# Kernel optimization log

Hardware: AMD Instinct MI355X
Metric: run time of the kernel (lower is better)

The kernel has to match this reference:

```python
import jax, jax.numpy as jnp
import numpy as np

DIM = 128
B, NQ, NK = 4, 4096, 4096
SCALE = DIM ** -0.5


def setup_inputs() -> dict:
    key = jax.random.key(0)
    ks = jax.random.split(key, 13)
    def lin(k, shape, scale=0.02):
        return jax.random.normal(k, shape, dtype=jnp.float32) * scale
    return {
        "query": jax.random.normal(ks[0], (B, NQ, DIM), dtype=jnp.float32),
        "key": jax.random.normal(ks[1], (B, NK, DIM), dtype=jnp.float32),
        "value": jax.random.normal(ks[2], (B, NK, DIM), dtype=jnp.float32),
        "att_bias": jax.random.normal(ks[3], (B, NK), dtype=jnp.float32),
        # params, [in, out] layout (torch Linear is x @ W.T + b)
        "q_w": lin(ks[4], (DIM, DIM)), "q_b": jnp.zeros((DIM,), jnp.float32),
        "k_w": lin(ks[5], (DIM, DIM)),
        "v_w": lin(ks[6], (DIM, DIM)), "v_b": jnp.zeros((DIM,), jnp.float32),
        "vs_w": lin(ks[7], (DIM, 1)), "vs_b": jnp.zeros((1,), jnp.float32),
        "p_w": lin(ks[8], (DIM, DIM)), "p_b": jnp.zeros((DIM,), jnp.float32),
    }


def reference(query, key, value, att_bias, q_w, q_b, k_w, v_w, v_b, vs_w, vs_b, p_w, p_b):
    # projections
    q = query @ q_w + q_b                      # [B, NQ, D]
    k = key @ k_w                              # [B, NK, D] (no bias)
    v = value @ v_w + v_b                      # [B, NK, D]
    # per-key semantic scalar, broadcast over queries: [B, 1, NK]
    semantic = (value @ vs_w + vs_b).reshape(value.shape[0], 1, value.shape[1])
    # scores + biases
    attn = jnp.einsum('bqd,bkd->bqk', q, k) * SCALE + semantic
    attn = attn + att_bias[:, None, :]
    attn = jax.nn.softmax(attn, axis=-1)
    out = jnp.einsum('bqk,bkd->bqd', attn, v)  # [B, NQ, D]
    out = out @ p_w + p_b
    return out
```

## Files before the change

### kernel.cpp

```cpp
#include <hip/hip_runtime.h>

typedef __bf16 bf16x8 __attribute__((ext_vector_type(8)));
typedef float f32x4 __attribute__((ext_vector_type(4)));
typedef float f32x16 __attribute__((ext_vector_type(16)));

#define MFMA16(a,b,c) __builtin_amdgcn_mfma_f32_16x16x32_bf16(a,b,c,0,0,0)
#define MFMA32(a,b,c) __builtin_amdgcn_mfma_f32_32x32x16_bf16(a,b,c,0,0,0)

static __device__ __forceinline__ unsigned short f2bf(float f){
  union{float f;unsigned u;}v; v.f=f;
  unsigned u=v.u;
  u += 0x7fffu + ((u>>16)&1u);
  return (unsigned short)(u>>16);
}
static __device__ __forceinline__ float bf2f(unsigned short h){
  union{unsigned u;float f;}v; v.u=((unsigned)h)<<16; return v.f;
}
static __device__ __forceinline__ unsigned cvtpk(float lo, float hi){
  unsigned r;
  asm("v_cvt_pk_bf16_f32 %0, %1, %2" : "=v"(r) : "v"(lo), "v"(hi));
  return r;
}
static __device__ __forceinline__ void gload16(const void* g, void* l){
  __builtin_amdgcn_global_load_lds(
    (const __attribute__((address_space(1))) unsigned int*)(uintptr_t)g,
    (__attribute__((address_space(3))) unsigned int*)(uintptr_t)l,
    16, 0, 0);
}

#define SCALE_QK 0.08838834764831845f
#define LOG2E    1.44269504088896340f
#define THR_L2   11.541560327111708f

#define SWZ128(r,c) (((r)<<7) + ((c) ^ (((r)&7)<<3)))


__global__ __launch_bounds__(256) void k_proj(
    const float* __restrict__ query, const float* __restrict__ key,
    const float* __restrict__ value, const float* __restrict__ att_bias,
    const float* __restrict__ q_w, const float* __restrict__ q_b,
    const float* __restrict__ k_w, const float* __restrict__ v_w,
    const float* __restrict__ v_b, const float* __restrict__ vs_w,
    const float* __restrict__ vs_b,
    unsigned short* __restrict__ qp, unsigned short* __restrict__ kp,
    unsigned short* __restrict__ vpt, float* __restrict__ biasc)
{
  const int t = blockIdx.y;
  const float* X = (t==0) ? query : ((t==1) ? key : value);
  const float* W = (t==0) ? q_w  : ((t==1) ? k_w : v_w);
  const int tid = threadIdx.x;
  const int row0 = blockIdx.x * 64;

  __shared__ __align__(16) unsigned short Wt[128][136];
  __shared__ __align__(16) unsigned short Xs[64][136];
  __shared__ float vsw_s[128];

  #pragma unroll 4
  for (int i=0;i<16;i++){
    int idx = tid*64 + i*4;
    float4 v4 = *(const float4*)(W + idx);
    Wt[(idx+0)&127][(idx+0)>>7] = f2bf(v4.x);
    Wt[(idx+1)&127][(idx+1)>>7] = f2bf(v4.y);
    Wt[(idx+2)&127][(idx+2)>>7] = f2bf(v4.z);
    Wt[(idx+3)&127][(idx+3)>>7] = f2bf(v4.w);
  }
  {
    const float* Xb = X + (size_t)row0*128;
    #pragma unroll
    for (int i=0;i<8;i++){
      int f4 = i*256 + tid;
      int row = f4>>5, c4 = f4&31;
      float4 v = *(const float4*)(Xb + row*128 + c4*4);
      ushort4 h;
      h.x = f2bf(v.x); h.y = f2bf(v.y); h.z = f2bf(v.z); h.w = f2bf(v.w);
      *(ushort4*)&Xs[row][c4*4] = h;
    }
  }
  if (t==2 && tid<128) vsw_s[tid] = vs_w[tid];
  __syncthreads();

  const int w = tid>>6, lane = tid&63, lr = lane&15, lg = lane>>4;
  f32x4 acc[8];
  #pragma unroll
  for (int nt=0;nt<8;nt++) acc[nt] = (f32x4){0.f,0.f,0.f,0.f};
  #pragma unroll
  for (int kk=0;kk<4;kk++){
    bf16x8 a = *(const bf16x8*)&Xs[w*16+lr][kk*32+lg*8];
    #pragma unroll
    for (int nt=0;nt<8;nt++){
      bf16x8 bb = *(const bf16x8*)&Wt[nt*16+lr][kk*32+lg*8];
      acc[nt] = MFMA16(a,bb,acc[nt]);
    }
  }

  if (t < 2){
    const float* bias = (t==0) ? q_b : (const float*)nullptr;
    const float sc = (t==0) ? (SCALE_QK*LOG2E) : 1.f;
    unsigned short* dstm = (t==0) ? qp : kp;
    #pragma unroll
    for (int nt=0;nt<8;nt++){
      int col = nt*16+lr;
      float bv = bias ? bias[col] : 0.f;
      #pragma unroll
      for (int r=0;r<4;r++){
        int row = row0 + w*16 + lg*4 + r;
        dstm[(size_t)row*128+col] = f2bf((acc[nt][r] + bv) * sc);
      }
    }
  } else {
    {
      int rl = tid>>2, part = tid&3;
      float s = 0.f;
      #pragma unroll
      for (int j=0;j<32;j++){
        int d = part*32+j;
        s += bf2f(Xs[rl][d]) * vsw_s[d];
      }
      s += __shfl_xor(s,1);
      s += __shfl_xor(s,2);
      if ((tid&3)==0){
        int rg = row0 + rl;
        biasc[rg] = (s + vs_b[0] + att_bias[rg]) * LOG2E;
      }
    }
    __syncthreads();
    unsigned short* Vls = (unsigned short*)Wt;
    #pragma unroll
    for (int nt=0;nt<8;nt++){
      int col = nt*16+lr;
      float bv = v_b[col];
      #pragma unroll
      for (int r=0;r<4;r++){
        int rl_ = w*16 + lg*4 + r;
        int k5 = rl_ & 31;
        int pos = 16*(k5>>4) + (k5&3) + 4*((k5>>3)&1) + 8*((k5>>2)&1);
        int np = (rl_ & 32) | pos;
        Vls[col*72 + np] = f2bf(acc[nt][r] + bv);
      }
    }
    __syncthreads();
    int d = tid>>1, half = tid&1;
    int bi = row0>>12, n0 = row0&4095;
    unsigned short* dst = vpt + ((size_t)(bi*128+d))*4096 + n0 + half*32;
    const unsigned short* src = Vls + d*72 + half*32;
    #pragma unroll
    for (int i=0;i<4;i++)
      *(uint4*)(dst + i*8) = *(const uint4*)(src + i*8);
  }
}

__global__ __launch_bounds__(256,3) void k_flash(
    const unsigned short* __restrict__ qp, const unsigned short* __restrict__ kp,
    const unsigned short* __restrict__ vpt, const float* __restrict__ biasc,
    unsigned short* __restrict__ opart, float* __restrict__ ml)
{
  const int f = blockIdx.x;
  const int xcd = f & 7, slot = f >> 3;
  const int group = xcd*4 + (slot>>5);
  const int b = group>>3, split = group&7;
  const int q0 = (slot & 31) * 128;

  const int tid = threadIdx.x;
  const int w = tid>>6, lane = tid&63;
  const int l31 = lane&31, hi = lane>>5;

  __shared__ __align__(16) unsigned short Ks[2][32*128];
  __shared__ __align__(16) char Vp[2][8192];
  __shared__ __align__(16) float Bs[512];

  const unsigned short* kbase = kp  + (size_t)(b*4096 + split*512)*128;
  const char* vbase = (const char*)(vpt + (size_t)b*128*4096 + split*512);
  const float* bbase = biasc + b*4096 + split*512;

  if (w < 2) gload16(bbase + w*256 + lane*4, (char*)Bs + w*1024);

  bf16x8 qf[8];
  {
    const unsigned short* qrow = qp + ((size_t)(b*4096 + q0 + w*32 + l31))*128;
    #pragma unroll
    for (int kk=0;kk<8;kk++) qf[kk] = *(const bf16x8*)(qrow + kk*16 + hi*8);
  }

  #define STAGE(bf_, k0_) do{                                                 \
    const char* kb_ = (const char*)kbase + (size_t)(k0_)*256;                 \
    const char* vb_ = vbase + (size_t)(k0_)*2;                                \
    _Pragma("unroll")                                                         \
    for (int i=0;i<2;i++){                                                    \
      int s_ = w*2+i;                                                         \
      int kr = s_*4 + (lane>>4);                                              \
      gload16(kb_ + kr*256 + (((lane&15)*16) ^ ((kr&7)*16)),                  \
              (char*)Ks[bf_] + s_*1024);                                      \
      int u_ = (lane&7) ^ ((lane>>3)&7);                                      \
      int vd = s_*16 + ((lane>>3)<<1) + (u_>>2);                              \
      gload16(vb_ + (size_t)vd*8192 + ((u_&3)<<4),                            \
              (char*)Vp[bf_] + s_*1024);                                      \
    }                                                                         \
  }while(0)

  float m_run = -INFINITY, l_run = 0.f;
  f32x16 acc[4];
  #pragma unroll
  for (int dt=0;dt<4;dt++) acc[dt] = (f32x16){};

  STAGE(0, 0);
  __syncthreads();

  const int vA = (l31>>1)*128;
  const int vX = ((l31>>1)&7)<<4;
  const int vH = (l31&1)*64 + hi*16;

  for (int t=0;t<16;t++){
    const int cur = t & 1;
    if (t<15) STAGE(cur^1, (t+1)*32);

    const unsigned short* Kc = Ks[cur];
    const char* Vc = Vp[cur];

    f32x16 sc = {};
    __builtin_amdgcn_s_setprio(1);
    #pragma unroll
    for (int kk=0;kk<8;kk++){
      bf16x8 a = *(const bf16x8*)&Kc[SWZ128(l31, kk*16 + hi*8)];
      sc = MFMA32(a, qf[kk], sc);
    }
    __builtin_amdgcn_s_setprio(0);

    const float* Bt = &Bs[t*32];
    float4 b0 = *(const float4*)&Bt[hi*4];
    float4 b1 = *(const float4*)&Bt[8 + hi*4];
    float4 b2 = *(const float4*)&Bt[16 + hi*4];
    float4 b3 = *(const float4*)&Bt[24 + hi*4];
    float tmax = -1e30f;
    #pragma unroll
    for (int c=0;c<4;c++){
      sc[c]    += ((const float*)&b0)[c];
      sc[4+c]  += ((const float*)&b1)[c];
      sc[8+c]  += ((const float*)&b2)[c];
      sc[12+c] += ((const float*)&b3)[c];
    }
    #pragma unroll
    for (int i=0;i<16;i++) tmax = fmaxf(tmax, sc[i]);
    tmax = fmaxf(tmax, __shfl_xor(tmax, 32));

    if (!__all(tmax <= m_run + THR_L2)){
      float mn = fmaxf(m_run, tmax);
      float corr = __builtin_exp2f(m_run - mn);
      m_run = mn;
      l_run *= corr;
      #pragma unroll
      for (int r=0;r<16;r++){
        int qn = (r&3) + 8*(r>>2) + 4*hi;
        float ca = __shfl(corr, qn);
        acc[0][r]*=ca; acc[1][r]*=ca; acc[2][r]*=ca; acc[3][r]*=ca;
      }
    }

    float rs = 0.f;
    #pragma unroll
    for (int i=0;i<16;i++){
      sc[i] = __builtin_exp2f(sc[i]-m_run); rs += sc[i];
    }
    rs += __shfl_xor(rs, 32);
    l_run += rs;

    {
      union { unsigned u[4]; bf16x8 v; } pu0;
      pu0.u[0] = cvtpk(sc[0], sc[1]);
      pu0.u[1] = cvtpk(sc[2], sc[3]);
      pu0.u[2] = cvtpk(sc[4], sc[5]);
      pu0.u[3] = cvtpk(sc[6], sc[7]);
      __builtin_amdgcn_s_setprio(1);
      #pragma unroll
      for (int dt=0;dt<4;dt++){
        bf16x8 v0 = *(const bf16x8*)(Vc + dt*2048 + vA + ((vH +  0) ^ vX));
        acc[dt] = MFMA32(pu0.v, v0, acc[dt]);
      }
      __builtin_amdgcn_s_setprio(0);
    }
    {
      union { unsigned u[4]; bf16x8 v; } pu1;
      pu1.u[0] = cvtpk(sc[8],  sc[9]);
      pu1.u[1] = cvtpk(sc[10], sc[11]);
      pu1.u[2] = cvtpk(sc[12], sc[13]);
      pu1.u[3] = cvtpk(sc[14], sc[15]);
      __builtin_amdgcn_s_setprio(1);
      #pragma unroll
      for (int dt=0;dt<4;dt++){
        bf16x8 v1 = *(const bf16x8*)(Vc + dt*2048 + vA + ((vH + 32) ^ vX));
        acc[dt] = MFMA32(pu1.v, v1, acc[dt]);
      }
      __builtin_amdgcn_s_setprio(0);
    }

    __syncthreads();
  }
  #undef STAGE

  const size_t rowbase = (size_t)split*16384 + (size_t)b*4096 + q0;
  #pragma unroll
  for (int r=0;r<16;r++){
    int qn = (r&3) + 8*(r>>2) + 4*hi;
    float inv = 1.f/__shfl(l_run, qn);
    size_t row = rowbase + w*32 + qn;
    opart[row*128 +      l31] = f2bf(acc[0][r]*inv);
    opart[row*128 + 32 + l31] = f2bf(acc[1][r]*inv);
    opart[row*128 + 64 + l31] = f2bf(acc[2][r]*inv);
    opart[row*128 + 96 + l31] = f2bf(acc[3][r]*inv);
  }
  if (hi==0){
    size_t rg = rowbase + w*32 + l31;
    ml[rg*2]   = m_run;
    ml[rg*2+1] = l_run;
  }
}

__global__ __launch_bounds__(256) void k_outproj(
    const unsigned short* __restrict__ opart, const float* __restrict__ ml,
    const float* __restrict__ p_w, const float* __restrict__ p_b,
    float* __restrict__ out)
{
  const int tid = threadIdx.x;
  const int row0 = blockIdx.x*32;
  __shared__ __align__(16) unsigned short Wt[128][136];
  __shared__ __align__(16) unsigned short Xs[32][136];
  __shared__ float wmg[8][32];

  #pragma unroll 4
  for (int i=0;i<16;i++){
    int idx = tid*64 + i*4;
    float4 v4 = *(const float4*)(p_w + idx);
    Wt[(idx+0)&127][(idx+0)>>7] = f2bf(v4.x);
    Wt[(idx+1)&127][(idx+1)>>7] = f2bf(v4.y);
    Wt[(idx+2)&127][(idx+2)>>7] = f2bf(v4.z);
    Wt[(idx+3)&127][(idx+3)>>7] = f2bf(v4.w);
  }
  if (tid < 32){
    int row = row0 + tid;
    float m[8], l[8];
    #pragma unroll
    for (int i=0;i<8;i++){
      m[i] = ml[((size_t)i*16384 + row)*2];
      l[i] = ml[((size_t)i*16384 + row)*2 + 1];
    }
    float M = m[0];
    #pragma unroll
    for (int i=1;i<8;i++) M = fmaxf(M, m[i]);
    float wi[8], wsum = 0.f;
    #pragma unroll
    for (int i=0;i<8;i++){ wi[i] = __builtin_exp2f(m[i]-M)*l[i]; wsum += wi[i]; }
    float inv = 1.f/wsum;
    #pragma unroll
    for (int i=0;i<8;i++) wmg[i][tid] = wi[i]*inv;
  }
  __syncthreads();
  #pragma unroll
  for (int i=0;i<2;i++){
    int e = (i*256 + tid)*8;
    int row = e>>7, col = e&127;
    float a8[8];
    #pragma unroll
    for (int j=0;j<8;j++) a8[j] = 0.f;
    #pragma unroll
    for (int s=0;s<8;s++){
      uint4 v = *(const uint4*)(opart + ((size_t)s*16384 + row0 + row)*128 + col);
      float wv = wmg[s][row];
      const unsigned short* hp = (const unsigned short*)&v;
      #pragma unroll
      for (int j=0;j<8;j++) a8[j] += wv * bf2f(hp[j]);
    }
    unsigned short h8[8];
    #pragma unroll
    for (int j=0;j<8;j++) h8[j] = f2bf(a8[j]);
    *(uint4*)&Xs[row][col] = *(const uint4*)h8;
  }
  __syncthreads();

  const int w=tid>>6, lane=tid&63, lr=lane&15, lg=lane>>4;
  const int r0 = (w&1)*16, c0 = (w>>1)*64;
  f32x4 acc[4];
  #pragma unroll
  for (int nt=0;nt<4;nt++) acc[nt] = (f32x4){0.f,0.f,0.f,0.f};
  #pragma unroll
  for (int kk=0;kk<4;kk++){
    bf16x8 a = *(const bf16x8*)&Xs[r0+lr][kk*32+lg*8];
    #pragma unroll
    for (int nt=0;nt<4;nt++){
      bf16x8 bb = *(const bf16x8*)&Wt[c0+nt*16+lr][kk*32+lg*8];
      acc[nt] = MFMA16(a,bb,acc[nt]);
    }
  }
  __syncthreads();
  float* Os = (float*)Wt;
  #pragma unroll
  for (int nt=0;nt<4;nt++){
    int col = c0 + nt*16 + lr;
    float pb = p_b[col];
    #pragma unroll
    for (int r=0;r<4;r++){
      int row = r0 + lg*4 + r;
      Os[row*132 + col] = acc[nt][r] + pb;
    }
  }
  __syncthreads();
  {
    int row = tid>>3, seg = tid&7;
    const float* src = Os + row*132 + seg*16;
    float* dst = out + (size_t)(row0+row)*128 + seg*16;
    #pragma unroll
    for (int i=0;i<4;i++)
      *(float4*)(dst + i*4) = *(const float4*)(src + i*4);
  }
}

extern "C" void kernel_launch(void* const* d_in, const int* in_sizes, int n_in,
                              void* d_out, int out_size, void* d_ws, size_t ws_size,
                              hipStream_t stream) {
  (void)in_sizes; (void)n_in; (void)out_size; (void)ws_size;
  const float* query    = (const float*)d_in[0];
  const float* key      = (const float*)d_in[1];
  const float* value    = (const float*)d_in[2];
  const float* att_bias = (const float*)d_in[3];
  const float* q_w = (const float*)d_in[4];
  const float* q_b = (const float*)d_in[5];
  const float* k_w = (const float*)d_in[6];
  const float* v_w = (const float*)d_in[7];
  const float* v_b = (const float*)d_in[8];
  const float* vs_w = (const float*)d_in[9];
  const float* vs_b = (const float*)d_in[10];
  const float* p_w = (const float*)d_in[11];
  const float* p_b = (const float*)d_in[12];

  char* ws = (char*)d_ws;
  unsigned short* qp    = (unsigned short*)(ws);
  unsigned short* kp    = (unsigned short*)(ws + 4194304);
  unsigned short* vpt   = (unsigned short*)(ws + 8388608);
  float*          biasc = (float*)(ws + 12582912);
  unsigned short* opart = (unsigned short*)(ws + 12648448);
  float*          ml    = (float*)(ws + 46202880);

  hipLaunchKernelGGL(k_proj, dim3(256,3), dim3(256), 0, stream,
    query,key,value,att_bias,q_w,q_b,k_w,v_w,v_b,vs_w,vs_b,qp,kp,vpt,biasc);
  hipLaunchKernelGGL(k_flash, dim3(1024), dim3(256), 0, stream,
    qp,kp,vpt,biasc,opart,ml);
  hipLaunchKernelGGL(k_outproj, dim3(512), dim3(256), 0, stream,
    opart,ml,p_w,p_b,(float*)d_out);
}
```

Before: 85.90 us.

## Process two 32-row query tiles per wave to reuse K/V fragments

Each wave now handles 64 query rows as two independent 32-row tiles, each with its own softmax state, so every K and V fragment read from LDS feeds two MFMAs. The query block grows to 256 rows and the grid halves to 512 blocks, which cuts K/V staging traffic per query. The cost is doubled accumulator and Q-fragment registers, with occupancy lowered to 2 blocks per SIMD, and fewer blocks to fill the 256 CUs.

```diff
diff --git a/kernel.cpp b/kernel.cpp
--- a/kernel.cpp
+++ b/kernel.cpp
@@ -149,16 +149,16 @@
   }
 }
 
-__global__ __launch_bounds__(256,3) void k_flash(
+__global__ __launch_bounds__(256,2) void k_flash(
     const unsigned short* __restrict__ qp, const unsigned short* __restrict__ kp,
     const unsigned short* __restrict__ vpt, const float* __restrict__ biasc,
     unsigned short* __restrict__ opart, float* __restrict__ ml)
 {
   const int f = blockIdx.x;
   const int xcd = f & 7, slot = f >> 3;
-  const int group = xcd*4 + (slot>>5);
+  const int group = xcd*4 + (slot>>4);
   const int b = group>>3, split = group&7;
-  const int q0 = (slot & 31) * 128;
+  const int q0 = (slot & 15) * 256;
 
   const int tid = threadIdx.x;
   const int w = tid>>6, lane = tid&63;
@@ -174,11 +174,15 @@
 
   if (w < 2) gload16(bbase + w*256 + lane*4, (char*)Bs + w*1024);
 
-  bf16x8 qf[8];
+  bf16x8 qfa[8], qfb[8];
   {
-    const unsigned short* qrow = qp + ((size_t)(b*4096 + q0 + w*32 + l31))*128;
-    #pragma unroll
-    for (int kk=0;kk<8;kk++) qf[kk] = *(const bf16x8*)(qrow + kk*16 + hi*8);
+    const unsigned short* qra = qp + ((size_t)(b*4096 + q0 + w*64 + l31))*128;
+    const unsigned short* qrb = qra + 32*128;
+    #pragma unroll
+    for (int kk=0;kk<8;kk++){
+      qfa[kk] = *(const bf16x8*)(qra + kk*16 + hi*8);
+      qfb[kk] = *(const bf16x8*)(qrb + kk*16 + hi*8);
+    }
   }
 
   #define STAGE(bf_, k0_) do{                                                 \
@@ -197,10 +201,10 @@
     }                                                                         \
   }while(0)
 
-  float m_run = -INFINITY, l_run = 0.f;
-  f32x16 acc[4];
-  #pragma unroll
-  for (int dt=0;dt<4;dt++) acc[dt] = (f32x16){};
+  float m_a = -INFINITY, l_a = 0.f, m_b = -INFINITY, l_b = 0.f;
+  f32x16 acca[4], accb[4];
+  #pragma unroll
+  for (int dt=0;dt<4;dt++){ acca[dt] = (f32x16){}; accb[dt] = (f32x16){}; }
 
   STAGE(0, 0);
   __syncthreads();
@@ -216,12 +220,13 @@
     const unsigned short* Kc = Ks[cur];
     const char* Vc = Vp[cur];
 
-    f32x16 sc = {};
+    f32x16 sca = {}, scb = {};
     __builtin_amdgcn_s_setprio(1);
     #pragma unroll
     for (int kk=0;kk<8;kk++){
       bf16x8 a = *(const bf16x8*)&Kc[SWZ128(l31, kk*16 + hi*8)];
-      sc = MFMA32(a, qf[kk], sc);
+      sca = MFMA32(a, qfa[kk], sca);
+      scb = MFMA32(a, qfb[kk], scb);
     }
     __builtin_amdgcn_s_setprio(0);
 
@@ -230,67 +235,70 @@
     float4 b1 = *(const float4*)&Bt[8 + hi*4];
     float4 b2 = *(const float4*)&Bt[16 + hi*4];
     float4 b3 = *(const float4*)&Bt[24 + hi*4];
-    float tmax = -1e30f;
+    float tma = -1e30f, tmb = -1e30f;
     #pragma unroll
     for (int c=0;c<4;c++){
-      sc[c]    += ((const float*)&b0)[c];
-      sc[4+c]  += ((const float*)&b1)[c];
-      sc[8+c]  += ((const float*)&b2)[c];
-      sc[12+c] += ((const float*)&b3)[c];
-    }
-    #pragma unroll
-    for (int i=0;i<16;i++) tmax = fmaxf(tmax, sc[i]);
-    tmax = fmaxf(tmax, __shfl_xor(tmax, 32));
-
-    if (!__all(tmax <= m_run + THR_L2)){
-      float mn = fmaxf(m_run, tmax);
-      float corr = __builtin_exp2f(m_run - mn);
-      m_run = mn;
-      l_run *= corr;
+      float bb0=((const float*)&b0)[c], bb1=((const float*)&b1)[c];
+      float bb2=((const float*)&b2)[c], bb3=((const float*)&b3)[c];
+      sca[c]+=bb0; sca[4+c]+=bb1; sca[8+c]+=bb2; sca[12+c]+=bb3;
+      scb[c]+=bb0; scb[4+c]+=bb1; scb[8+c]+=bb2; scb[12+c]+=bb3;
+    }
+    #pragma unroll
+    for (int i=0;i<16;i++){ tma = fmaxf(tma, sca[i]); tmb = fmaxf(tmb, scb[i]); }
+    tma = fmaxf(tma, __shfl_xor(tma, 32));
+    tmb = fmaxf(tmb, __shfl_xor(tmb, 32));
+
+    if (!__all(tma <= m_a + THR_L2)){
+      float mn = fmaxf(m_a, tma);
+      float corr = __builtin_exp2f(m_a - mn);
+      m_a = mn; l_a *= corr;
       #pragma unroll
       for (int r=0;r<16;r++){
-        int qn = (r&3) + 8*(r>>2) + 4*hi;
-        float ca = __shfl(corr, qn);
-        acc[0][r]*=ca; acc[1][r]*=ca; acc[2][r]*=ca; acc[3][r]*=ca;
-      }
-    }
-
-    float rs = 0.f;
+        float ca = __shfl(corr, (r&3) + 8*(r>>2) + 4*hi);
+        acca[0][r]*=ca; acca[1][r]*=ca; acca[2][r]*=ca; acca[3][r]*=ca;
+      }
+    }
+    if (!__all(tmb <= m_b + THR_L2)){
+      float mn = fmaxf(m_b, tmb);
+      float corr = __builtin_exp2f(m_b - mn);
+      m_b = mn; l_b *= corr;
+      #pragma unroll
+      for (int r=0;r<16;r++){
+        float cb = __shfl(corr, (r&3) + 8*(r>>2) + 4*hi);
+        accb[0][r]*=cb; accb[1][r]*=cb; accb[2][r]*=cb; accb[3][r]*=cb;
+      }
+    }
+
+    float rsa = 0.f, rsb = 0.f;
     #pragma unroll
     for (int i=0;i<16;i++){
-      sc[i] = __builtin_exp2f(sc[i]-m_run); rs += sc[i];
-    }
-    rs += __shfl_xor(rs, 32);
-    l_run += rs;
-
-    {
-      union { unsigned u[4]; bf16x8 v; } pu0;
-      pu0.u[0] = cvtpk(sc[0], sc[1]);
-      pu0.u[1] = cvtpk(sc[2], sc[3]);
-      pu0.u[2] = cvtpk(sc[4], sc[5]);
-      pu0.u[3] = cvtpk(sc[6], sc[7]);
-      __builtin_amdgcn_s_setprio(1);
-      #pragma unroll
-      for (int dt=0;dt<4;dt++){
-        bf16x8 v0 = *(const bf16x8*)(Vc + dt*2048 + vA + ((vH +  0) ^ vX));
-        acc[dt] = MFMA32(pu0.v, v0, acc[dt]);
-      }
-      __builtin_amdgcn_s_setprio(0);
-    }
-    {
-      union { unsigned u[4]; bf16x8 v; } pu1;
-      pu1.u[0] = cvtpk(sc[8],  sc[9]);
-      pu1.u[1] = cvtpk(sc[10], sc[11]);
-      pu1.u[2] = cvtpk(sc[12], sc[13]);
-      pu1.u[3] = cvtpk(sc[14], sc[15]);
-      __builtin_amdgcn_s_setprio(1);
-      #pragma unroll
-      for (int dt=0;dt<4;dt++){
-        bf16x8 v1 = *(const bf16x8*)(Vc + dt*2048 + vA + ((vH + 32) ^ vX));
-        acc[dt] = MFMA32(pu1.v, v1, acc[dt]);
-      }
-      __builtin_amdgcn_s_setprio(0);
-    }
+      sca[i] = __builtin_exp2f(sca[i]-m_a); rsa += sca[i];
+      scb[i] = __builtin_exp2f(scb[i]-m_b); rsb += scb[i];
+    }
+    rsa += __shfl_xor(rsa, 32); l_a += rsa;
+    rsb += __shfl_xor(rsb, 32); l_b += rsb;
+
+    union { unsigned u[4]; bf16x8 v; } p0a, p1a, p0b, p1b;
+    p0a.u[0]=cvtpk(sca[0], sca[1]);  p0a.u[1]=cvtpk(sca[2], sca[3]);
+    p0a.u[2]=cvtpk(sca[4], sca[5]);  p0a.u[3]=cvtpk(sca[6], sca[7]);
+    p1a.u[0]=cvtpk(sca[8], sca[9]);  p1a.u[1]=cvtpk(sca[10],sca[11]);
+    p1a.u[2]=cvtpk(sca[12],sca[13]); p1a.u[3]=cvtpk(sca[14],sca[15]);
+    p0b.u[0]=cvtpk(scb[0], scb[1]);  p0b.u[1]=cvtpk(scb[2], scb[3]);
+    p0b.u[2]=cvtpk(scb[4], scb[5]);  p0b.u[3]=cvtpk(scb[6], scb[7]);
+    p1b.u[0]=cvtpk(scb[8], scb[9]);  p1b.u[1]=cvtpk(scb[10],scb[11]);
+    p1b.u[2]=cvtpk(scb[12],scb[13]); p1b.u[3]=cvtpk(scb[14],scb[15]);
+
+    __builtin_amdgcn_s_setprio(1);
+    #pragma unroll
+    for (int dt=0;dt<4;dt++){
+      bf16x8 v0 = *(const bf16x8*)(Vc + dt*2048 + vA + ((vH +  0) ^ vX));
+      acca[dt] = MFMA32(p0a.v, v0, acca[dt]);
+      accb[dt] = MFMA32(p0b.v, v0, accb[dt]);
+      bf16x8 v1 = *(const bf16x8*)(Vc + dt*2048 + vA + ((vH + 32) ^ vX));
+      acca[dt] = MFMA32(p1a.v, v1, acca[dt]);
+      accb[dt] = MFMA32(p1b.v, v1, accb[dt]);
+    }
+    __builtin_amdgcn_s_setprio(0);
 
     __syncthreads();
   }
@@ -300,17 +308,26 @@
   #pragma unroll
   for (int r=0;r<16;r++){
     int qn = (r&3) + 8*(r>>2) + 4*hi;
-    float inv = 1.f/__shfl(l_run, qn);
-    size_t row = rowbase + w*32 + qn;
-    opart[row*128 +      l31] = f2bf(acc[0][r]*inv);
-    opart[row*128 + 32 + l31] = f2bf(acc[1][r]*inv);
-    opart[row*128 + 64 + l31] = f2bf(acc[2][r]*inv);
-    opart[row*128 + 96 + l31] = f2bf(acc[3][r]*inv);
+    float ia = 1.f/__shfl(l_a, qn);
+    float ib = 1.f/__shfl(l_b, qn);
+    size_t ra = rowbase + w*64 + qn;
+    size_t rb = ra + 32;
+    opart[ra*128 +      l31] = f2bf(acca[0][r]*ia);
+    opart[ra*128 + 32 + l31] = f2bf(acca[1][r]*ia);
+    opart[ra*128 + 64 + l31] = f2bf(acca[2][r]*ia);
+    opart[ra*128 + 96 + l31] = f2bf(acca[3][r]*ia);
+    opart[rb*128 +      l31] = f2bf(accb[0][r]*ib);
+    opart[rb*128 + 32 + l31] = f2bf(accb[1][r]*ib);
+    opart[rb*128 + 64 + l31] = f2bf(accb[2][r]*ib);
+    opart[rb*128 + 96 + l31] = f2bf(accb[3][r]*ib);
   }
   if (hi==0){
-    size_t rg = rowbase + w*32 + l31;
-    ml[rg*2]   = m_run;
-    ml[rg*2+1] = l_run;
+    size_t rga = rowbase + w*64 + l31;
+    size_t rgb = rga + 32;
+    ml[rga*2]   = m_a;
+    ml[rga*2+1] = l_a;
+    ml[rgb*2]   = m_b;
+    ml[rgb*2+1] = l_b;
   }
 }
 
@@ -440,7 +457,7 @@
 
   hipLaunchKernelGGL(k_proj, dim3(256,3), dim3(256), 0, stream,
     query,key,value,att_bias,q_w,q_b,k_w,v_w,v_b,vs_w,vs_b,qp,kp,vpt,biasc);
-  hipLaunchKernelGGL(k_flash, dim3(1024), dim3(256), 0, stream,
+  hipLaunchKernelGGL(k_flash, dim3(512), dim3(256), 0, stream,
     qp,kp,vpt,biasc,opart,ml);
   hipLaunchKernelGGL(k_outproj, dim3(512), dim3(256), 0, stream,
     opart,ml,p_w,p_b,(float*)d_out);
```

Result: slower. 88.80 us (+3.4%).
